# Optimization experiments

Hardware: AMD Instinct MI355X
Metric: run time of the kernel (lower is better)

Reference implementation:

```python
import jax, jax.numpy as jnp
from jax import lax
import numpy as np

ALPHA = 0.5; EPS = 1e-6; RANK_PAIRS = 100
W_MEAN = 0.5; W_STD = 0.5
L_STAT = 1.0; L_RANK = 1.0; L_SMOOTH = 1.0
LABELS = np.array([5, 8, 13], dtype=np.int32)
TGT_CV = np.array([0.077, 0.227, 0.348], dtype=np.float32)


def _erode(mask_f):
    # torch: 1 - max_pool2d(1-x, k=3, pad=1); implicit -inf padding means
    # out-of-bounds pixels act as foreground -> min-pool with +inf init.
    return lax.reduce_window(mask_f, jnp.inf, lax.min, (3, 3), (1, 1), 'SAME') > 0.5


def _per_region(pred, pix, region, tgt_cv, key):
    # pred, pix: [H,W] float; region: [H,W] bool
    H, W = pred.shape
    HW = H * W
    regf = region.astype(jnp.float32)
    e1 = _erode(regf)
    e2 = _erode(e1.astype(jnp.float32))  # erode(region, iterations=2)
    core1 = jnp.where(jnp.sum(e1) < 2, region, e1)
    core2 = jnp.where(jnp.sum(e2) < 3, core1, e2)
    n_reg = jnp.sum(region)

    # ---- std (coefficient-of-variation) term on core2
    c2 = core2.astype(jnp.float32)
    n2 = jnp.sum(c2)
    n2s = jnp.maximum(n2, 1.0)
    mu = jnp.sum(pred * c2) / n2s
    var = jnp.sum(c2 * (pred - mu) ** 2) / n2s  # unbiased=False
    cv = jnp.sqrt(var) / (jnp.abs(mu) + EPS)
    std_val = jnp.abs(cv - tgt_cv)
    std_valid = (n_reg >= 3) & (n2 >= 3)

    # ---- pairwise rank term on core1 (sampled-pair path; realistic regions
    # always have n > full_pair_threshold=20)
    c1f = core1.reshape(-1).astype(jnp.float32)
    n1 = jnp.sum(c1f)
    p = jnp.where(n1 > 0, c1f / jnp.maximum(n1, 1.0), 1.0 / HW)
    k1, k2 = jax.random.split(key)
    ii = jax.random.choice(k1, HW, (RANK_PAIRS,), replace=True, p=p)
    jj = jax.random.choice(k2, HW, (RANK_PAIRS,), replace=True, p=p)
    pf = pred.reshape(-1)
    xf = pix.reshape(-1)
    s = jnp.sign(xf[ii] - xf[jj])
    pv = ((ii != jj) & (s != 0)).astype(jnp.float32)
    hinge = jax.nn.relu(-(pf[ii] - pf[jj]) * s)
    npv = jnp.sum(pv)
    rank_val = jnp.sum(hinge * pv) / jnp.maximum(npv, 1.0)
    rank_valid = (n_reg >= 2) & (n1 >= 2) & (npv > 0)

    # ---- smoothness term on core2
    dx = jnp.abs(pred[:, 1:] - pred[:, :-1])
    mx = (core2[:, 1:] & core2[:, :-1]).astype(jnp.float32)
    dy = jnp.abs(pred[1:, :] - pred[:-1, :])
    my = (core2[1:, :] & core2[:-1, :]).astype(jnp.float32)
    cx = jnp.sum(mx); cy = jnp.sum(my)
    mean_x = jnp.sum(dx * mx) / jnp.maximum(cx, 1.0)
    mean_y = jnp.sum(dy * my) / jnp.maximum(cy, 1.0)
    hx = (cx > 0).astype(jnp.float32); hy = (cy > 0).astype(jnp.float32)
    npres = hx + hy
    smooth_val = (mean_x * hx + mean_y * hy) / jnp.maximum(npres, 1.0)
    smooth_valid = (n_reg >= 3) & (n2 >= 3) & (npres > 0)

    return std_val, std_valid, rank_val, rank_valid, smooth_val, smooth_valid


def _masked_mean(v, valid):
    vf = valid.astype(jnp.float32)
    c = jnp.sum(vf)
    return jnp.where(c > 0, jnp.sum(v * vf) / jnp.maximum(c, 1.0), 0.0)


def _forward(pred, target, lab14, img1, img2):
    B, _, H, W = pred.shape
    p2 = pred[:, 0]
    lab = lab14[:, 0]
    t1 = img1[:, 0]
    t2 = img2[:, 0]
    pix = (1.0 - ALPHA) * (1.0 - t1) + ALPHA * t2  # pixel_map
    loss_mean = jnp.mean(jnp.abs(pred - target))

    labels = jnp.asarray(LABELS)
    regions = lab[:, None, :, :] == labels[None, :, None, None]  # [B,3,H,W]
    R = regions.reshape(B * 3, H, W)
    P = jnp.broadcast_to(p2[:, None], (B, 3, H, W)).reshape(B * 3, H, W)
    X = jnp.broadcast_to(pix[:, None], (B, 3, H, W)).reshape(B * 3, H, W)
    T = jnp.tile(jnp.asarray(TGT_CV), B)  # [B*3], label-minor matches reshape
    keys = jax.random.split(jax.random.key(42), B * 3)

    sv, svd, rv, rvd, mv, mvd = jax.vmap(_per_region)(P, X, R, T, keys)
    loss_std = _masked_mean(sv, svd)
    loss_rank = _masked_mean(rv, rvd)
    loss_smooth = _masked_mean(mv, mvd)

    loss_stat = W_MEAN * loss_mean + W_STD * loss_std
    return L_STAT * loss_stat + L_RANK * loss_rank + L_SMOOTH * loss_smooth


def setup_inputs() -> dict:
    key = jax.random.key(0)
    k1, k2, k3, k4, k5 = jax.random.split(key, 5)
    B, H, W = 16, 512, 512
    pred = jax.random.normal(k1, (B, 1, H, W), dtype=jnp.float32)
    target = jax.random.normal(k2, (B, 1, H, W), dtype=jnp.float32)
    lab14 = jax.random.randint(k3, (B, 1, H, W), 0, 15, dtype=jnp.int32)
    img1 = jax.random.uniform(k4, (B, 1, H, W), dtype=jnp.float32)
    img2 = jax.random.uniform(k5, (B, 1, H, W), dtype=jnp.float32)
    return {"pred": pred, "target": target, "lab14": lab14, "img1": img1, "img2": img2}


def reference(pred, target, lab14, img1, img2):
    return _forward(pred, target, lab14, img1, img2)
```

## Files before the change

### kernel.cpp

```cpp
#include <hip/hip_runtime.h>

#define BB 16
#define HH 512
#define WW 512
#define BH 8
#define NR (BH+5)
#define NBANDS (HH/BH)
#define NREG 48
#define HWTOT (HH*WW)
#define MASK13 0x1FFFu

#define OFF_SUMABS 4608
#define OFF_COUNTS 4616
#define OFF_RANKV  6344
#define OFF_RANKD  6536
#define OFF_CTR    6728
#define OFF_ROWCR  8192
#define OFF_ROWCE  (OFF_ROWCR + 48*512*4)
#define OFF_MREG   (OFF_ROWCE + 48*512*4)
#define MASKBYTES  (48LL*512*8*8)
#define OFF_ME1    (OFF_MREG + MASKBYTES)

__device__ __forceinline__ unsigned int hashu(unsigned int x) {
  x ^= x >> 16; x *= 0x7feb352dU; x ^= x >> 15; x *= 0x846ca68bU; x ^= x >> 16;
  return x;
}

__global__ __launch_bounds__(512, 4) void pass1_kernel(
    const float* __restrict__ pred, const float* __restrict__ target,
    const int* __restrict__ lab,
    double* __restrict__ sums, double* __restrict__ sumAbs,
    int* __restrict__ counts,
    unsigned long long* __restrict__ mRegG, unsigned long long* __restrict__ mE1G,
    int* __restrict__ rowcR, int* __restrict__ rowcE)
{
  __shared__ unsigned long long XCH[514];
  __shared__ unsigned long long NB0[512];
  __shared__ unsigned int      NB2[512];
  __shared__ int   RC[48];
  __shared__ float RED[8][37];
  __shared__ unsigned int CNT[8][14];

  const int t    = threadIdx.x;
  const int lane = t & 63;
  const int wv   = t >> 6;
  const int c    = t;
  const int r0   = blockIdx.x * BH;
  const int b    = blockIdx.y;
  const int R    = r0 - 3;

  if (t < 48) RC[t] = 0;

  unsigned int OOR = 0;
  {
    int topClip = -R;
    if (topClip > 0) OOR |= (1u << topClip) - 1u;
    int botStart = HH - R;
    if (botStart < NR) OOR |= (~0u << botStart) & ((1u << NR) - 1u);
  }

  unsigned int colm0 = 0, colm1 = 0, colm2 = 0;
  #pragma unroll
  for (int lr = 0; lr < NR; ++lr) {
    int gy = R + lr;
    if ((unsigned)gy < (unsigned)HH) {
      int l = lab[((size_t)b*HH + gy)*WW + c];
      colm0 |= (l == 5)  ? (1u << lr) : 0u;
      colm1 |= (l == 8)  ? (1u << lr) : 0u;
      colm2 |= (l == 13) ? (1u << lr) : 0u;
    }
  }

  unsigned long long pk =  (unsigned long long)(colm0 | OOR)
        | ((unsigned long long)(colm1 | OOR) << 13)
        | ((unsigned long long)(colm2 | OOR) << 26);
  XCH[c+1] = pk;
  if (t == 0) { XCH[0] = ~0ull; XCH[513] = ~0ull; }
  __syncthreads();
  unsigned long long hp = pk & XCH[c] & XCH[c+2];
  unsigned int e1a[3];
  #pragma unroll
  for (int li = 0; li < 3; ++li) {
    unsigned int h = (unsigned int)((hp >> (13*li)) & MASK13);
    e1a[li] = h & (h >> 1) & (h << 1);
  }
  __syncthreads();
  unsigned long long pk2 =  (unsigned long long)((e1a[0] | OOR) & MASK13)
        | ((unsigned long long)((e1a[1] | OOR) & MASK13) << 13)
        | ((unsigned long long)((e1a[2] | OOR) & MASK13) << 26);
  XCH[c+1] = pk2;
  __syncthreads();
  unsigned long long hp2 = pk2 & XCH[c] & XCH[c+2];
  unsigned int e2a[3];
  #pragma unroll
  for (int li = 0; li < 3; ++li) {
    unsigned int h = (unsigned int)((hp2 >> (13*li)) & MASK13);
    e2a[li] = h & (h >> 1) & (h << 1);
  }

  unsigned int mS[9] = { colm0, e1a[0], e2a[0],
                         colm1, e1a[1], e2a[1],
                         colm2, e1a[2], e2a[2] };

  {
    unsigned long long p0 = 0;
    #pragma unroll
    for (int cb = 0; cb < 8; ++cb) p0 |= (unsigned long long)((mS[cb] >> 3) & 0xFFu) << (cb*8);
    NB0[c] = p0; NB2[c] = (mS[8] >> 3) & 0xFFu;
  }
  __syncthreads();
  unsigned long long nb0 = (c < 511) ? NB0[c+1] : 0ull;
  unsigned int       nb2 = (c < 511) ? NB2[c+1] : 0u;

  {
    unsigned int pkc[14];
    #pragma unroll
    for (int j = 0; j < 14; ++j) pkc[j] = 0;
    #pragma unroll
    for (int cb = 0; cb < 9; ++cb) {
      unsigned int w8 = (mS[cb] >> 3) & 0xFFu;
      unsigned int nbw;
      if (cb < 8) nbw = (unsigned int)(nb0 >> (cb*8)) & 0xFFu;
      else        nbw = nb2 & 0xFFu;
      unsigned int mcl = mS[cb] & ~OOR;
      unsigned int q   = mcl & (mcl << 1);
      unsigned int cnt = __popc(w8);
      unsigned int cx  = __popc(w8 & nbw);
      unsigned int cy  = __popc((q >> 3) & 0xFFu);
      int k0 = cb*3;
      pkc[(k0  )>>1] |= cnt << (((k0  )&1)*16);
      pkc[(k0+1)>>1] |= cx  << (((k0+1)&1)*16);
      pkc[(k0+2)>>1] |= cy  << (((k0+2)&1)*16);
    }
    #pragma unroll
    for (int j = 0; j < 14; ++j) {
      unsigned int v = pkc[j];
      for (int off = 32; off; off >>= 1) v += __shfl_down(v, off);
      if (lane == 0) CNT[wv][j] = v;
    }
  }

  #pragma unroll
  for (int row = 0; row < BH; ++row) {
    int lr = row + 3, gy = r0 + row;
    #pragma unroll
    for (int li = 0; li < 3; ++li) {
      unsigned long long wR = __ballot((mS[li*3]   >> lr) & 1u);
      unsigned long long wE = __ballot((mS[li*3+1] >> lr) & 1u);
      if (lane == 0) {
        size_t base = (((size_t)(b*3 + li))*HH + gy)*8 + wv;
        mRegG[base] = wR; mE1G[base] = wE;
        atomicAdd(&RC[     li*BH + row], (int)__popcll(wR));
        atomicAdd(&RC[24 + li*BH + row], (int)__popcll(wE));
      }
    }
  }

  float aP[9] = {}, aP2[9] = {}, aDX[9] = {}, aDY[9] = {};
  float aAbs = 0.f;
  const float* pB = pred   + (size_t)b*HH*WW;
  const float* tB = target + (size_t)b*HH*WW;
  float p_prev = (r0 > 0) ? pB[(size_t)(r0-1)*WW + c] : 0.f;
  const int cR = (c < 511) ? c + 1 : c;

  #pragma unroll
  for (int row = 0; row < BH; ++row) {
    const int lr = row + 3, gy = r0 + row;
    const float* prow = pB + (size_t)gy*WW;
    float p  = prow[c];
    float pr = prow[cR];
    float tg = tB[(size_t)gy*WW + c];
    aAbs += fabsf(p - tg);
    float d = fabsf(pr - p);
    float v = (gy > 0) ? fabsf(p - p_prev) : 0.f;
    #pragma unroll
    for (int cb = 0; cb < 9; ++cb) {
      unsigned int cur = mS[cb];
      unsigned int c1 = (cur >> lr) & 1u;
      unsigned int u1 = (cur >> (lr-1)) & 1u;
      unsigned int r1;
      if (cb < 8) r1 = (unsigned int)(nb0 >> (cb*8 + row)) & 1u;
      else        r1 = (nb2 >> row) & 1u;
      float f = c1 ? p : 0.f;
      aP[cb]  += f;
      aP2[cb]  = fmaf(f, p, aP2[cb]);
      aDX[cb] += (c1 & r1) ? d : 0.f;
      aDY[cb] += (c1 & u1) ? v : 0.f;
    }
    p_prev = p;
  }

  #pragma unroll
  for (int cb = 0; cb < 9; ++cb) {
    float s0 = aP[cb], s1 = aP2[cb], s2 = aDX[cb], s3 = aDY[cb];
    for (int off = 32; off; off >>= 1) {
      s0 += __shfl_down(s0, off);
      s1 += __shfl_down(s1, off);
      s2 += __shfl_down(s2, off);
      s3 += __shfl_down(s3, off);
    }
    if (lane == 0) {
      RED[wv][0*9 + cb] = s0; RED[wv][1*9 + cb] = s1;
      RED[wv][2*9 + cb] = s2; RED[wv][3*9 + cb] = s3;
    }
  }
  {
    float va = aAbs;
    for (int off = 32; off; off >>= 1) va += __shfl_down(va, off);
    if (lane == 0) RED[wv][36] = va;
  }
  __syncthreads();

  if (t < 37) {
    float s = 0.f;
    #pragma unroll
    for (int w = 0; w < 8; ++w) s += RED[w][t];
    if (t < 36) {
      int stat = t / 9, cb = t % 9, li = cb / 3, m = cb % 3;
      atomicAdd(sums + (size_t)(b*3 + li)*12 + stat*3 + m, (double)s);
    } else {
      atomicAdd(sumAbs, (double)s);
    }
  }
  if (t < 14) {
    unsigned int s = 0;
    #pragma unroll
    for (int w = 0; w < 8; ++w) s += CNT[w][t];
    int k0 = t*2;
    #pragma unroll
    for (int h = 0; h < 2; ++h) {
      int k = k0 + h;
      if (k < 27) {
        unsigned int val = (s >> (h*16)) & 0xFFFFu;
        int cb = k / 3, stat = k % 3, li = cb / 3, m = cb % 3;
        atomicAdd(counts + (b*3 + li)*9 + stat*3 + m, (int)val);
      }
    }
  }
  if (t < 48) {
    int type = t / 24, rem = t % 24;
    int li = rem / BH, row = rem % BH, gy = r0 + row;
    int* dst = type ? rowcE : rowcR;
    dst[((size_t)(b*3 + li))*HH + gy] = RC[t];
  }
}

__global__ __launch_bounds__(256) void pass2_kernel(
    const float* __restrict__ pred, const float* __restrict__ img1,
    const float* __restrict__ img2,
    const unsigned long long* __restrict__ mRegG,
    const unsigned long long* __restrict__ mE1G,
    const int* __restrict__ rowcR, const int* __restrict__ rowcE,
    const int* __restrict__ counts,
    const double* __restrict__ sums, const double* __restrict__ sumAbs,
    float* __restrict__ rankval, int* __restrict__ rankvalid,
    int* __restrict__ ctr, float* __restrict__ out)
{
  const int r = blockIdx.x;
  const int b = r / 3;
  const int t = threadIdx.x;
  const int lane = t & 63;
  const int wv   = t >> 6;
  __shared__ int rowc[HH];
  __shared__ int pre[HH];
  __shared__ int grpPre[64];
  __shared__ int idxArr[200];
  __shared__ float redH[4];
  __shared__ int   redP[4];
  __shared__ int lastFlag;
  __shared__ double svvS[NREG], smvS[NREG];
  __shared__ int svdS[NREG], smdS[NREG];
  __shared__ float rkvS[NREG];
  __shared__ int   rkdS[NREG];

  int n_reg = counts[r*9 + 0];
  int n_e1  = counts[r*9 + 1];
  int useE1 = (n_e1 >= 2);
  int n1 = useE1 ? n_e1 : n_reg;
  bool doRank = (n_reg >= 2 && n1 >= 2);
  float rv = 0.f; int rvd = 0;

  if (doRank) {
    const int* rc = (useE1 ? rowcE : rowcR) + (size_t)r*HH;
    { int2 vv = ((const int2*)rc)[t]; rowc[2*t] = vv.x; rowc[2*t+1] = vv.y; }
    __syncthreads();
    if (t < 64) {
      int base = t*8, s = 0;
      #pragma unroll
      for (int k = 0; k < 8; ++k) s += rowc[base + k];
      int v = s;
      for (int off = 1; off < 64; off <<= 1) {
        int o = __shfl_up(v, off);
        if (t >= off) v += o;
      }
      grpPre[t] = v - s;
    }
    __syncthreads();
    if (t < 64) {
      int s = grpPre[t], base = t*8;
      #pragma unroll
      for (int k = 0; k < 8; ++k) { pre[base + k] = s; s += rowc[base + k]; }
    }
    __syncthreads();

    const unsigned long long* M = (useE1 ? mE1G : mRegG) + (size_t)r*HH*8;
    if (t < 200) {
      unsigned int h = hashu(0x9e3779b9u + (unsigned)(r*200 + t));
      float u = (float)(h >> 8) * (1.0f / 16777216.0f);
      int k = (int)(u * (float)n1);
      if (k >= n1) k = n1 - 1;
      if (k < 0) k = 0;
      int lo = 0, hi = HH;
      while (hi - lo > 1) { int mid = (lo + hi) >> 1; if (pre[mid] <= k) lo = mid; else hi = mid; }
      int row = lo;
      int local = k - pre[row];
      int idx = 0;
      #pragma unroll
      for (int w = 0; w < 8; ++w) {
        unsigned long long mm = M[row*8 + w];
        int cc = __popcll(mm);
        if (local < cc) {
          for (int i = 0; i < local; ++i) mm &= mm - 1;
          idx = row*WW + w*64 + __builtin_ctzll(mm);
          local = 1 << 20;
        } else {
          local -= cc;
        }
      }
      idxArr[t] = idx;
    }
    __syncthreads();

    float hv = 0.f; int pv = 0;
    if (t < 100) {
      int ii = idxArr[t], jj = idxArr[t+100];
      size_t base = (size_t)b * HWTOT;
      float pi = pred[base+ii], pj = pred[base+jj];
      float xi = 0.5f*(1.f - img1[base+ii]) + 0.5f*img2[base+ii];
      float xj = 0.5f*(1.f - img1[base+jj]) + 0.5f*img2[base+jj];
      float s = (xi > xj) ? 1.f : ((xi < xj) ? -1.f : 0.f);
      pv = (ii != jj) && (s != 0.f);
      float hinge = fmaxf(0.f, -(pi - pj)*s);
      hv = pv ? hinge : 0.f;
    }
    for (int off = 32; off; off >>= 1) {
      hv += __shfl_down(hv, off);
      pv += __shfl_down(pv, off);
    }
    if (lane == 0) { redH[wv] = hv; redP[wv] = pv; }
    __syncthreads();
    if (t == 0) {
      float sh = redH[0] + redH[1] + redH[2] + redH[3];
      int   sp = redP[0] + redP[1] + redP[2] + redP[3];
      rv  = sh / (float)(sp > 0 ? sp : 1);
      rvd = (sp > 0) ? 1 : 0;
    }
  }

  if (t == 0) {
    atomicExch(&rankval[r], rv);
    atomicExch(&rankvalid[r], rvd);
    __threadfence();
    int old = atomicAdd(ctr, 1);
    lastFlag = (old == NREG - 1);
  }
  __syncthreads();

  if (lastFlag) {
    __threadfence();
    if (t < NREG) {
      int li = t % 3;
      const int* C = counts + t*9;
      const double* S = sums + (size_t)t*12;
      int nr = C[0], ne1 = C[1], ne2 = C[2];
      int m1 = (ne1 < 2) ? 0 : 1;
      int m2 = (ne2 < 3) ? m1 : 2;
      int n2 = C[m2];
      double n2s = (double)(n2 > 1 ? n2 : 1);
      double mu  = S[m2] / n2s;
      double var = S[3+m2] / n2s - mu*mu;
      if (var < 0.0) var = 0.0;
      double cv = sqrt(var) / (fabs(mu) + 1e-6);
      double tcv = (li == 0) ? 0.077 : ((li == 1) ? 0.227 : 0.348);
      svvS[t] = fabs(cv - tcv);
      svdS[t] = (nr >= 3 && n2 >= 3);
      int cx = C[3+m2], cy = C[6+m2];
      double mean_x = S[6+m2] / (double)(cx > 1 ? cx : 1);
      double mean_y = S[9+m2] / (double)(cy > 1 ? cy : 1);
      int hx = (cx > 0), hy = (cy > 0);
      int npres = hx + hy;
      smvS[t] = (mean_x*hx + mean_y*hy) / (double)(npres > 1 ? npres : 1);
      smdS[t] = (nr >= 3 && n2 >= 3 && npres > 0);
      rkvS[t] = rankval[t];
      rkdS[t] = rankvalid[t];
    }
    __syncthreads();
    if (t == 0) {
      double s_std = 0, s_sm = 0, s_rk = 0;
      int c_std = 0, c_sm = 0, c_rk = 0;
      for (int i = 0; i < NREG; ++i) {
        if (svdS[i]) { s_std += svvS[i]; c_std++; }
        if (smdS[i]) { s_sm  += smvS[i]; c_sm++;  }
        if (rkdS[i]) { s_rk  += rkvS[i]; c_rk++;  }
      }
      double loss_std = c_std ? s_std / c_std : 0.0;
      double loss_sm  = c_sm  ? s_sm  / c_sm  : 0.0;
      double loss_rk  = c_rk  ? s_rk  / c_rk  : 0.0;
      double loss_mean = sumAbs[0] / (double)((long long)BB * HWTOT);
      double total = 0.5*loss_mean + 0.5*loss_std + loss_rk + loss_sm;
      out[0] = (float)total;
    }
  }
}

extern "C" void kernel_launch(void* const* d_in, const int* in_sizes, int n_in,
                              void* d_out, int out_size, void* d_ws, size_t ws_size,
                              hipStream_t stream) {
  const float* pred   = (const float*)d_in[0];
  const float* target = (const float*)d_in[1];
  const int*   lab    = (const int*)d_in[2];
  const float* img1   = (const float*)d_in[3];
  const float* img2   = (const float*)d_in[4];
  float* out = (float*)d_out;
  char* ws = (char*)d_ws;

  double* sums    = (double*)ws;
  double* sumAbs  = (double*)(ws + OFF_SUMABS);
  int*    counts  = (int*)(ws + OFF_COUNTS);
  float*  rankval = (float*)(ws + OFF_RANKV);
  int*    rankvld = (int*)(ws + OFF_RANKD);
  int*    ctr     = (int*)(ws + OFF_CTR);
  int*    rowcR   = (int*)(ws + OFF_ROWCR);
  int*    rowcE   = (int*)(ws + OFF_ROWCE);
  unsigned long long* mReg = (unsigned long long*)(ws + OFF_MREG);
  unsigned long long* mE1  = (unsigned long long*)(ws + OFF_ME1);

  hipMemsetAsync(ws, 0, 8192, stream);

  dim3 g1(NBANDS, BB);
  pass1_kernel<<<g1, 512, 0, stream>>>(pred, target, lab, sums, sumAbs, counts,
                                       mReg, mE1, rowcR, rowcE);
  pass2_kernel<<<NREG, 256, 0, stream>>>(pred, img1, img2, mReg, mE1, rowcR, rowcE,
                                         counts, sums, sumAbs, rankval, rankvld, ctr, out);
}
```

Before: 167.4 us.

## Replace global atomics with per-block partials and drop memset launch

Pass 1 now writes per-band partial sums and counts to dedicated slots instead of issuing double-precision global atomics, and pass 2 reduces those partials per region. The hipMemsetAsync launch is removed by having one pass-1 block reset the completion counter. The per-row ballot loop with shared atomics is replaced by precomputed packed masks and a single lane-indexed ballot store, and row counts are now recomputed in pass 2 by popcounting the masks. Accumulation moves from double to float partials, which risks small precision differences, and clearing the counter inside pass 1 relies on stream ordering with the previous pass 2.

```diff
diff --git a/kernel.cpp b/kernel.cpp
--- a/kernel.cpp
+++ b/kernel.cpp
@@ -6,18 +6,19 @@
 #define BH 8
 #define NR (BH+5)
 #define NBANDS (HH/BH)
+#define NBLK (NBANDS*BB)
 #define NREG 48
 #define HWTOT (HH*WW)
 #define MASK13 0x1FFFu
 
-#define OFF_SUMABS 4608
-#define OFF_COUNTS 4616
-#define OFF_RANKV  6344
-#define OFF_RANKD  6536
-#define OFF_CTR    6728
-#define OFF_ROWCR  8192
-#define OFF_ROWCE  (OFF_ROWCR + 48*512*4)
-#define OFF_MREG   (OFF_ROWCE + 48*512*4)
+#define OFF_CNT48  0
+#define OFF_SUM48  2048
+#define OFF_RANKV  4608
+#define OFF_RANKD  4800
+#define OFF_CTR    5120
+#define OFF_SUMSP  8192
+#define OFF_CNTP   (OFF_SUMSP + NBLK*40*4)
+#define OFF_MREG   (OFF_CNTP + NBLK*28*4)
 #define MASKBYTES  (48LL*512*8*8)
 #define OFF_ME1    (OFF_MREG + MASKBYTES)
 
@@ -29,15 +30,13 @@
 __global__ __launch_bounds__(512, 4) void pass1_kernel(
     const float* __restrict__ pred, const float* __restrict__ target,
     const int* __restrict__ lab,
-    double* __restrict__ sums, double* __restrict__ sumAbs,
-    int* __restrict__ counts,
+    float* __restrict__ sumsP, int* __restrict__ countsP,
     unsigned long long* __restrict__ mRegG, unsigned long long* __restrict__ mE1G,
-    int* __restrict__ rowcR, int* __restrict__ rowcE)
+    int* __restrict__ ctr)
 {
   __shared__ unsigned long long XCH[514];
   __shared__ unsigned long long NB0[512];
   __shared__ unsigned int      NB2[512];
-  __shared__ int   RC[48];
   __shared__ float RED[8][37];
   __shared__ unsigned int CNT[8][14];
 
@@ -48,8 +47,9 @@
   const int r0   = blockIdx.x * BH;
   const int b    = blockIdx.y;
   const int R    = r0 - 3;
-
-  if (t < 48) RC[t] = 0;
+  const int bandblk = b * NBANDS + blockIdx.x;
+
+  if (blockIdx.x == 0 && b == 0 && t == 0) *ctr = 0;
 
   unsigned int OOR = 0;
   {
@@ -112,21 +112,44 @@
   unsigned long long nb0 = (c < 511) ? NB0[c+1] : 0ull;
   unsigned int       nb2 = (c < 511) ? NB2[c+1] : 0u;
 
+  unsigned int W[9];
+  const unsigned int nOOR = ~OOR;
+  #pragma unroll
+  for (int cb = 0; cb < 9; ++cb) {
+    unsigned int w8  = (mS[cb] >> 3) & 0xFFu;
+    unsigned int nbw = (cb < 8) ? ((unsigned int)(nb0 >> (cb*8)) & 0xFFu) : (nb2 & 0xFFu);
+    unsigned int px8 = w8 & nbw;
+    unsigned int mcl = mS[cb] & nOOR;
+    unsigned int py8 = ((mcl & (mcl << 1)) >> 3) & 0xFFu;
+    W[cb] = w8 | (px8 << 8) | (py8 << 16);
+  }
+
+  {
+    unsigned long long myWord = 0;
+    #pragma unroll
+    for (int k = 0; k < 48; ++k) {
+      const int ktype = k / 24, krem = k % 24, kli = krem >> 3, krow = krem & 7;
+      unsigned int bit = (W[kli*3 + ktype] >> krow) & 1u;
+      unsigned long long wrd = __ballot(bit != 0u);
+      if (lane == k) myWord = wrd;
+    }
+    if (lane < 48) {
+      int type = lane / 24, rem = lane % 24, li = rem >> 3, row = rem & 7;
+      int gy = r0 + row;
+      unsigned long long* dst = type ? mE1G : mRegG;
+      dst[(((size_t)(b*3 + li))*HH + gy)*8 + wv] = myWord;
+    }
+  }
+
   {
     unsigned int pkc[14];
     #pragma unroll
     for (int j = 0; j < 14; ++j) pkc[j] = 0;
     #pragma unroll
     for (int cb = 0; cb < 9; ++cb) {
-      unsigned int w8 = (mS[cb] >> 3) & 0xFFu;
-      unsigned int nbw;
-      if (cb < 8) nbw = (unsigned int)(nb0 >> (cb*8)) & 0xFFu;
-      else        nbw = nb2 & 0xFFu;
-      unsigned int mcl = mS[cb] & ~OOR;
-      unsigned int q   = mcl & (mcl << 1);
-      unsigned int cnt = __popc(w8);
-      unsigned int cx  = __popc(w8 & nbw);
-      unsigned int cy  = __popc((q >> 3) & 0xFFu);
+      unsigned int cnt = __popc(W[cb] & 0x0000FFu);
+      unsigned int cx  = __popc(W[cb] & 0x00FF00u);
+      unsigned int cy  = __popc(W[cb] & 0xFF0000u);
       int k0 = cb*3;
       pkc[(k0  )>>1] |= cnt << (((k0  )&1)*16);
       pkc[(k0+1)>>1] |= cx  << (((k0+1)&1)*16);
@@ -137,22 +160,6 @@
       unsigned int v = pkc[j];
       for (int off = 32; off; off >>= 1) v += __shfl_down(v, off);
       if (lane == 0) CNT[wv][j] = v;
-    }
-  }
-
-  #pragma unroll
-  for (int row = 0; row < BH; ++row) {
-    int lr = row + 3, gy = r0 + row;
-    #pragma unroll
-    for (int li = 0; li < 3; ++li) {
-      unsigned long long wR = __ballot((mS[li*3]   >> lr) & 1u);
-      unsigned long long wE = __ballot((mS[li*3+1] >> lr) & 1u);
-      if (lane == 0) {
-        size_t base = (((size_t)(b*3 + li))*HH + gy)*8 + wv;
-        mRegG[base] = wR; mE1G[base] = wE;
-        atomicAdd(&RC[     li*BH + row], (int)__popcll(wR));
-        atomicAdd(&RC[24 + li*BH + row], (int)__popcll(wE));
-      }
     }
   }
 
@@ -165,27 +172,24 @@
 
   #pragma unroll
   for (int row = 0; row < BH; ++row) {
-    const int lr = row + 3, gy = r0 + row;
+    const int gy = r0 + row;
     const float* prow = pB + (size_t)gy*WW;
     float p  = prow[c];
     float pr = prow[cR];
     float tg = tB[(size_t)gy*WW + c];
     aAbs += fabsf(p - tg);
     float d = fabsf(pr - p);
-    float v = (gy > 0) ? fabsf(p - p_prev) : 0.f;
+    float v = fabsf(p - p_prev);
     #pragma unroll
     for (int cb = 0; cb < 9; ++cb) {
-      unsigned int cur = mS[cb];
-      unsigned int c1 = (cur >> lr) & 1u;
-      unsigned int u1 = (cur >> (lr-1)) & 1u;
-      unsigned int r1;
-      if (cb < 8) r1 = (unsigned int)(nb0 >> (cb*8 + row)) & 1u;
-      else        r1 = (nb2 >> row) & 1u;
+      unsigned int c1 = (W[cb] >> row) & 1u;
+      unsigned int px = (W[cb] >> (row + 8)) & 1u;
+      unsigned int py = (W[cb] >> (row + 16)) & 1u;
       float f = c1 ? p : 0.f;
       aP[cb]  += f;
       aP2[cb]  = fmaf(f, p, aP2[cb]);
-      aDX[cb] += (c1 & r1) ? d : 0.f;
-      aDY[cb] += (c1 & u1) ? v : 0.f;
+      aDX[cb] += px ? d : 0.f;
+      aDY[cb] += py ? v : 0.f;
     }
     p_prev = p;
   }
@@ -215,33 +219,14 @@
     float s = 0.f;
     #pragma unroll
     for (int w = 0; w < 8; ++w) s += RED[w][t];
-    if (t < 36) {
-      int stat = t / 9, cb = t % 9, li = cb / 3, m = cb % 3;
-      atomicAdd(sums + (size_t)(b*3 + li)*12 + stat*3 + m, (double)s);
-    } else {
-      atomicAdd(sumAbs, (double)s);
-    }
+    sumsP[(size_t)bandblk*40 + t] = s;
   }
   if (t < 14) {
     unsigned int s = 0;
     #pragma unroll
     for (int w = 0; w < 8; ++w) s += CNT[w][t];
-    int k0 = t*2;
-    #pragma unroll
-    for (int h = 0; h < 2; ++h) {
-      int k = k0 + h;
-      if (k < 27) {
-        unsigned int val = (s >> (h*16)) & 0xFFFFu;
-        int cb = k / 3, stat = k % 3, li = cb / 3, m = cb % 3;
-        atomicAdd(counts + (b*3 + li)*9 + stat*3 + m, (int)val);
-      }
-    }
-  }
-  if (t < 48) {
-    int type = t / 24, rem = t % 24;
-    int li = rem / BH, row = rem % BH, gy = r0 + row;
-    int* dst = type ? rowcE : rowcR;
-    dst[((size_t)(b*3 + li))*HH + gy] = RC[t];
+    countsP[bandblk*28 + 2*t]     = (int)(s & 0xFFFFu);
+    countsP[bandblk*28 + 2*t + 1] = (int)(s >> 16);
   }
 }
 
@@ -250,17 +235,17 @@
     const float* __restrict__ img2,
     const unsigned long long* __restrict__ mRegG,
     const unsigned long long* __restrict__ mE1G,
-    const int* __restrict__ rowcR, const int* __restrict__ rowcE,
-    const int* __restrict__ counts,
-    const double* __restrict__ sums, const double* __restrict__ sumAbs,
+    const float* __restrict__ sumsP, const int* __restrict__ countsP,
+    int* __restrict__ counts48, float* __restrict__ sums48,
     float* __restrict__ rankval, int* __restrict__ rankvalid,
     int* __restrict__ ctr, float* __restrict__ out)
 {
   const int r = blockIdx.x;
-  const int b = r / 3;
+  const int b = r / 3, li = r % 3;
   const int t = threadIdx.x;
   const int lane = t & 63;
   const int wv   = t >> 6;
+  __shared__ int LC[9];
   __shared__ int rowc[HH];
   __shared__ int pre[HH];
   __shared__ int grpPre[64];
@@ -270,19 +255,50 @@
   __shared__ int lastFlag;
   __shared__ double svvS[NREG], smvS[NREG];
   __shared__ int svdS[NREG], smdS[NREG];
-  __shared__ float rkvS[NREG];
-  __shared__ int   rkdS[NREG];
-
-  int n_reg = counts[r*9 + 0];
-  int n_e1  = counts[r*9 + 1];
+  __shared__ double SAB[4];
+
+  if (t < 9) LC[t] = 0;
+  __syncthreads();
+  for (int k = t; k < 9*NBANDS; k += 256) {
+    int s9 = k >> 6, band = k & 63;
+    int m = s9 / 3, st = s9 % 3;
+    atomicAdd(&LC[s9], countsP[(b*NBANDS + band)*28 + (li*3 + m)*3 + st]);
+  }
+  if (wv == 0) {
+    float sp[12];
+    #pragma unroll
+    for (int j = 0; j < 12; ++j) {
+      int stat = j / 3, m = j % 3;
+      sp[j] = sumsP[(size_t)(b*NBANDS + lane)*40 + stat*9 + li*3 + m];
+    }
+    #pragma unroll
+    for (int j = 0; j < 12; ++j)
+      for (int off = 32; off; off >>= 1) sp[j] += __shfl_down(sp[j], off);
+    if (lane == 0) {
+      #pragma unroll
+      for (int j = 0; j < 12; ++j) atomicExch(&sums48[r*12 + j], sp[j]);
+    }
+  }
+  __syncthreads();
+  if (t < 9) atomicExch(&counts48[r*9 + t], LC[t]);
+
+  int n_reg = LC[0], n_e1 = LC[3];
   int useE1 = (n_e1 >= 2);
   int n1 = useE1 ? n_e1 : n_reg;
   bool doRank = (n_reg >= 2 && n1 >= 2);
   float rv = 0.f; int rvd = 0;
 
   if (doRank) {
-    const int* rc = (useE1 ? rowcE : rowcR) + (size_t)r*HH;
-    { int2 vv = ((const int2*)rc)[t]; rowc[2*t] = vv.x; rowc[2*t+1] = vv.y; }
+    const unsigned long long* M = (useE1 ? mE1G : mRegG) + (size_t)r*HH*8;
+    {
+      int row = t*2;
+      int c0 = 0, c1v = 0;
+      #pragma unroll
+      for (int w = 0; w < 8; ++w) c0 += __popcll(M[(size_t)row*8 + w]);
+      #pragma unroll
+      for (int w = 0; w < 8; ++w) c1v += __popcll(M[(size_t)(row+1)*8 + w]);
+      rowc[row] = c0; rowc[row+1] = c1v;
+    }
     __syncthreads();
     if (t < 64) {
       int base = t*8, s = 0;
@@ -303,7 +319,6 @@
     }
     __syncthreads();
 
-    const unsigned long long* M = (useE1 ? mE1G : mRegG) + (size_t)r*HH*8;
     if (t < 200) {
       unsigned int h = hashu(0x9e3779b9u + (unsigned)(r*200 + t));
       float u = (float)(h >> 8) * (1.0f / 16777216.0f);
@@ -317,7 +332,7 @@
       int idx = 0;
       #pragma unroll
       for (int w = 0; w < 8; ++w) {
-        unsigned long long mm = M[row*8 + w];
+        unsigned long long mm = M[(size_t)row*8 + w];
         int cc = __popcll(mm);
         if (local < cc) {
           for (int i = 0; i < local; ++i) mm &= mm - 1;
@@ -357,6 +372,7 @@
     }
   }
 
+  __syncthreads();
   if (t == 0) {
     atomicExch(&rankval[r], rv);
     atomicExch(&rankvalid[r], rvd);
@@ -368,47 +384,49 @@
 
   if (lastFlag) {
     __threadfence();
+    double pa = 0.0;
+    for (int k = t; k < NBLK; k += 256) pa += (double)sumsP[(size_t)k*40 + 36];
+    for (int off = 32; off; off >>= 1) pa += __shfl_down(pa, off);
+    if (lane == 0) SAB[wv] = pa;
     if (t < NREG) {
-      int li = t % 3;
-      const int* C = counts + t*9;
-      const double* S = sums + (size_t)t*12;
-      int nr = C[0], ne1 = C[1], ne2 = C[2];
+      const int* C = counts48 + t*9;
+      const float* S = sums48 + t*12;
+      int nr = C[0], ne1 = C[3], ne2 = C[6];
       int m1 = (ne1 < 2) ? 0 : 1;
       int m2 = (ne2 < 3) ? m1 : 2;
-      int n2 = C[m2];
+      int n2 = C[m2*3];
       double n2s = (double)(n2 > 1 ? n2 : 1);
-      double mu  = S[m2] / n2s;
-      double var = S[3+m2] / n2s - mu*mu;
+      double mu  = (double)S[m2] / n2s;
+      double var = (double)S[3+m2] / n2s - mu*mu;
       if (var < 0.0) var = 0.0;
       double cv = sqrt(var) / (fabs(mu) + 1e-6);
-      double tcv = (li == 0) ? 0.077 : ((li == 1) ? 0.227 : 0.348);
+      int tli = t % 3;
+      double tcv = (tli == 0) ? 0.077 : ((tli == 1) ? 0.227 : 0.348);
       svvS[t] = fabs(cv - tcv);
       svdS[t] = (nr >= 3 && n2 >= 3);
-      int cx = C[3+m2], cy = C[6+m2];
-      double mean_x = S[6+m2] / (double)(cx > 1 ? cx : 1);
-      double mean_y = S[9+m2] / (double)(cy > 1 ? cy : 1);
+      int cx = C[m2*3+1], cy = C[m2*3+2];
+      double mean_x = (double)S[6+m2] / (double)(cx > 1 ? cx : 1);
+      double mean_y = (double)S[9+m2] / (double)(cy > 1 ? cy : 1);
       int hx = (cx > 0), hy = (cy > 0);
       int npres = hx + hy;
       smvS[t] = (mean_x*hx + mean_y*hy) / (double)(npres > 1 ? npres : 1);
       smdS[t] = (nr >= 3 && n2 >= 3 && npres > 0);
-      rkvS[t] = rankval[t];
-      rkdS[t] = rankvalid[t];
     }
     __syncthreads();
     if (t == 0) {
       double s_std = 0, s_sm = 0, s_rk = 0;
       int c_std = 0, c_sm = 0, c_rk = 0;
       for (int i = 0; i < NREG; ++i) {
-        if (svdS[i]) { s_std += svvS[i]; c_std++; }
-        if (smdS[i]) { s_sm  += smvS[i]; c_sm++;  }
-        if (rkdS[i]) { s_rk  += rkvS[i]; c_rk++;  }
+        if (svdS[i])       { s_std += svvS[i];     c_std++; }
+        if (smdS[i])       { s_sm  += smvS[i];     c_sm++;  }
+        if (rankvalid[i])  { s_rk  += rankval[i];  c_rk++;  }
       }
       double loss_std = c_std ? s_std / c_std : 0.0;
       double loss_sm  = c_sm  ? s_sm  / c_sm  : 0.0;
       double loss_rk  = c_rk  ? s_rk  / c_rk  : 0.0;
-      double loss_mean = sumAbs[0] / (double)((long long)BB * HWTOT);
-      double total = 0.5*loss_mean + 0.5*loss_std + loss_rk + loss_sm;
-      out[0] = (float)total;
+      double loss_mean = (SAB[0] + SAB[1] + SAB[2] + SAB[3])
+                         / (double)((long long)BB * HWTOT);
+      out[0] = (float)(0.5*loss_mean + 0.5*loss_std + loss_rk + loss_sm);
     }
   }
 }
@@ -424,22 +442,20 @@
   float* out = (float*)d_out;
   char* ws = (char*)d_ws;
 
-  double* sums    = (double*)ws;
-  double* sumAbs  = (double*)(ws + OFF_SUMABS);
-  int*    counts  = (int*)(ws + OFF_COUNTS);
-  float*  rankval = (float*)(ws + OFF_RANKV);
-  int*    rankvld = (int*)(ws + OFF_RANKD);
-  int*    ctr     = (int*)(ws + OFF_CTR);
-  int*    rowcR   = (int*)(ws + OFF_ROWCR);
-  int*    rowcE   = (int*)(ws + OFF_ROWCE);
+  int*    counts48 = (int*)(ws + OFF_CNT48);
+  float*  sums48   = (float*)(ws + OFF_SUM48);
+  float*  rankval  = (float*)(ws + OFF_RANKV);
+  int*    rankvld  = (int*)(ws + OFF_RANKD);
+  int*    ctr      = (int*)(ws + OFF_CTR);
+  float*  sumsP    = (float*)(ws + OFF_SUMSP);
+  int*    countsP  = (int*)(ws + OFF_CNTP);
   unsigned long long* mReg = (unsigned long long*)(ws + OFF_MREG);
   unsigned long long* mE1  = (unsigned long long*)(ws + OFF_ME1);
 
-  hipMemsetAsync(ws, 0, 8192, stream);
-
   dim3 g1(NBANDS, BB);
-  pass1_kernel<<<g1, 512, 0, stream>>>(pred, target, lab, sums, sumAbs, counts,
-                                       mReg, mE1, rowcR, rowcE);
-  pass2_kernel<<<NREG, 256, 0, stream>>>(pred, img1, img2, mReg, mE1, rowcR, rowcE,
-                                         counts, sums, sumAbs, rankval, rankvld, ctr, out);
+  pass1_kernel<<<g1, 512, 0, stream>>>(pred, target, lab, sumsP, countsP,
+                                       mReg, mE1, ctr);
+  pass2_kernel<<<NREG, 256, 0, stream>>>(pred, img1, img2, mReg, mE1,
+                                         sumsP, countsP, counts48, sums48,
+                                         rankval, rankvld, ctr, out);
 }
```

New measurement: 167.7 us. About the same (+0.2%).
